# Kernel optimization log

Measured on AMD Instinct MI355X. Metric: run time of the kernel, lower is better.

Reference implementation:

```python
import jax, jax.numpy as jnp
import numpy as np

Nknn = 10
Np = 20
N = 524288
DOWN, LEFT, RIGHT, UP, WIDTH = -5.0, -5.0, 5.0, 5.0, 1.0


def setup_inputs() -> dict:
    key = jax.random.key(0)
    ks = jax.random.split(key, 20)
    def p(k, shape, fan_in):
        return jax.random.normal(k, shape, jnp.float32) / jnp.sqrt(jnp.float32(fan_in))
    inp = {
        "t": jax.random.uniform(ks[0], (1,), jnp.float32),
        "y": jax.random.normal(ks[1], (N, 4 + 2 * Np), jnp.float32),
        # net1: Linear(4,8) -> ReLU -> Linear(8,2)
        "w1a": p(ks[2], (4, 8), 4),   "b1a": p(ks[3], (8,), 4),
        "w1b": p(ks[4], (8, 2), 8),   "b1b": p(ks[5], (2,), 8),
        # net2: Linear(1,16) -> ReLU -> Linear(16,8) -> ReLU -> Linear(8,1)
        "w2a": p(ks[6], (1, 16), 1),  "b2a": p(ks[7], (16,), 1),
        "w2b": p(ks[8], (16, 8), 16), "b2b": p(ks[9], (8,), 16),
        "w2c": p(ks[10], (8, 1), 8),  "b2c": p(ks[11], (1,), 8),
        # net3: same architecture as net2
        "w3a": p(ks[12], (1, 16), 1), "b3a": p(ks[13], (16,), 1),
        "w3b": p(ks[14], (16, 8), 16),"b3b": p(ks[15], (8,), 16),
        "w3c": p(ks[16], (8, 1), 8),  "b3c": p(ks[17], (1,), 8),
    }
    return inp


def _mlp3(x, wa, ba, wb, bb, wc, bc):
    # Linear -> ReLU -> Linear -> ReLU -> Linear, applied on last axis
    h = jax.nn.relu(x @ wa + ba)
    h = jax.nn.relu(h @ wb + bb)
    return h @ wc + bc


def reference(t, y, w1a, b1a, w1b, b1b, w2a, b2a, w2b, b2b, w2c, b2c,
              w3a, b3a, w3b, b3b, w3c, b3c):
    y = y.astype(jnp.float32)
    theX = y[:, 0:2]            # positions [N,2]
    theV = y[:, 2:4]            # velocities [N,2]
    ux = y[:, 4:4 + 2 * Nknn].reshape(-1, Nknn, 2)  # neighbor offsets [N,Nknn,2]

    dxdt = theV

    # goal-attraction term f1
    door = jnp.array([RIGHT + 0.6, 0.0], jnp.float32)
    diff = door - theX
    unit_e = diff / jnp.sqrt(jnp.sum(diff * diff, axis=1, keepdims=True))
    h = jax.nn.relu(jnp.concatenate([unit_e, theV], axis=1) @ w1a + b1a)
    f1 = h @ w1b + b1b          # [N,2]

    # wall-repulsion term f2; rows inside the door gap get rightdist=100
    x0 = theX[:, 0:1]
    x1 = theX[:, 1:2]
    rightdist = jnp.where((x1 < WIDTH) & (x1 > -WIDTH), 100.0, RIGHT - x0)
    wall_in = jnp.stack([x0 - LEFT, x1 - DOWN, UP - x1, rightdist], axis=1)  # [N,4,1]
    o = _mlp3(wall_in, w2a, b2a, w2b, bb=b2b, wc=w2c, bc=b2c) if False else _mlp3(wall_in, w2a, b2a, w2b, b2b, w2c, b2c)  # [N,4,1]
    # directions: [1,0], [0,1], [0,-1], [-1,0]
    f2 = jnp.concatenate([o[:, 0] - o[:, 3], o[:, 1] - o[:, 2]], axis=1)  # [N,2]

    # neighbor-repulsion term f3 (vectorized over Nknn)
    d = jnp.sqrt(jnp.sum(ux * ux, axis=2, keepdims=True))  # [N,Nknn,1]
    f3 = -jnp.sum(_mlp3(d, w3a, b3a, w3b, b3b, w3c, b3c) * ux / d, axis=1)  # [N,2]

    dvdt = (f1 + f2 + f3) / 80.0
    dudt = jnp.zeros((y.shape[0], 2 * Nknn), y.dtype)
    result = jnp.concatenate([dxdt, dvdt, dudt], axis=1)  # [N, 4 + 2*Nknn]

    # zero out agents that have exited (x > RIGHT)
    result = jnp.where((theX[:, 0] > RIGHT)[:, None], 0.0, result)
    return result
```

## Files before the change

kernel.cpp:

```cpp
#include <hip/hip_runtime.h>

#define NROW  524288
#define BLK   256
#define TPB   2
#define NKNN  10
#define YCOLS 44
#define OCOLS 24

#define TBL    256
#define T2_LO  (-2.0f)
#define T3_LO  (0.0f)
#define T_H    (1.0f / 16.0f)
#define T_INVH 16.0f

typedef float f32x4 __attribute__((ext_vector_type(4)));

__device__ __forceinline__ float mlp_scalar_g(float s,
    const float* __restrict__ wa, const float* __restrict__ ba,
    const float* __restrict__ wb, const float* __restrict__ bb,
    const float* __restrict__ wc, const float* __restrict__ bc) {
    float h[16];
#pragma unroll
    for (int j = 0; j < 16; ++j)
        h[j] = fmaxf(fmaf(s, wa[j], ba[j]), 0.0f);
    float g[8];
#pragma unroll
    for (int k = 0; k < 8; ++k) g[k] = bb[k];
#pragma unroll
    for (int j = 0; j < 16; ++j) {
        float hj = h[j];
#pragma unroll
        for (int k = 0; k < 8; ++k)
            g[k] = fmaf(hj, wb[j * 8 + k], g[k]);
    }
    float o = bc[0];
#pragma unroll
    for (int k = 0; k < 8; ++k)
        o = fmaf(fmaxf(g[k], 0.0f), wc[k], o);
    return o;
}

__device__ __forceinline__ float tbl_eval(const float* __restrict__ T, float s, float lo) {
    float u = (s - lo) * T_INVH;
    u = fminf(fmaxf(u, 0.0f), (float)TBL - 1.001f);
    int i = (int)u;
    float f = u - (float)i;
    float va = T[i];
    float vb = T[i + 1];
    return fmaf(f, vb - va, va);
}

__device__ __forceinline__ void load_tile(const f32x4* __restrict__ yb,
                                          int w, int lane, f32x4 ld[6]) {
#pragma unroll
    for (int i = 0; i < 6; ++i) {
        int j  = lane + i * 64;
        int rr = j / 6;
        int cc = j - rr * 6;
        ld[i]  = yb[(64 * w + rr) * 11 + cc];
    }
}

__device__ __forceinline__ void stage_tile(f32x4* __restrict__ S,
                                           int w, int lane, const f32x4 ld[6]) {
#pragma unroll
    for (int i = 0; i < 6; ++i)
        S[384 * w + lane + i * 64] = ld[i];
}

__device__ __forceinline__ void compute_row(f32x4* __restrict__ S, int t,
    const float* __restrict__ T2v, const float* __restrict__ T3v, float o100,
    const float* __restrict__ w1a, const float* __restrict__ b1a,
    const float* __restrict__ w1b, const float* __restrict__ b1b)
{
    f32x4 a  = S[t * 6 + 0];
    f32x4 u0 = S[t * 6 + 1];
    f32x4 u1 = S[t * 6 + 2];
    f32x4 u2 = S[t * 6 + 3];
    f32x4 u3 = S[t * 6 + 4];
    f32x4 u4 = S[t * 6 + 5];

    float dx = 5.6f - a.x;
    float dy = 0.0f - a.y;
    float inv = rsqrtf(fmaf(dx, dx, dy * dy));
    float in1[4] = { dx * inv, dy * inv, a.z, a.w };
    float h1[8];
#pragma unroll
    for (int j = 0; j < 8; ++j) {
        float s = b1a[j];
#pragma unroll
        for (int k = 0; k < 4; ++k)
            s = fmaf(in1[k], w1a[k * 8 + j], s);
        h1[j] = fmaxf(s, 0.0f);
    }
    float f1x = b1b[0];
    float f1y = b1b[1];
#pragma unroll
    for (int j = 0; j < 8; ++j) {
        f1x = fmaf(h1[j], w1b[j * 2 + 0], f1x);
        f1y = fmaf(h1[j], w1b[j * 2 + 1], f1y);
    }

    bool corridor = (a.y < 1.0f) && (a.y > -1.0f);
    float o0 = tbl_eval(T2v, a.x + 5.0f, T2_LO);
    float o1 = tbl_eval(T2v, a.y + 5.0f, T2_LO);
    float o2 = tbl_eval(T2v, 5.0f - a.y, T2_LO);
    float o3 = corridor ? o100 : tbl_eval(T2v, 5.0f - a.x, T2_LO);
    float f2x = o0 - o3;
    float f2y = o1 - o2;

    float us[2 * NKNN] = { u0.x, u0.y, u0.z, u0.w,
                           u1.x, u1.y, u1.z, u1.w,
                           u2.x, u2.y, u2.z, u2.w,
                           u3.x, u3.y, u3.z, u3.w,
                           u4.x, u4.y, u4.z, u4.w };
    float f3x = 0.0f, f3y = 0.0f;
#pragma unroll
    for (int n = 0; n < NKNN; ++n) {
        float uxn = us[2 * n + 0];
        float uyn = us[2 * n + 1];
        float s2  = fmaf(uxn, uxn, uyn * uyn);
        float idn = rsqrtf(s2);
        float d   = s2 * idn;
        float m   = tbl_eval(T3v, d, T3_LO);
        float c   = m * idn;
        f3x = fmaf(-c, uxn, f3x);
        f3y = fmaf(-c, uyn, f3y);
    }

    bool dead = (a.x > 5.0f);
    const float k80 = 1.0f / 80.0f;
    f32x4 r;
    r.x = dead ? 0.0f : a.z;
    r.y = dead ? 0.0f : a.w;
    r.z = dead ? 0.0f : (f1x + f2x + f3x) * k80;
    r.w = dead ? 0.0f : (f1y + f2y + f3y) * k80;

    const f32x4 z = (f32x4)(0.0f);
    S[t * 6 + 0] = r;
    S[t * 6 + 1] = z;
    S[t * 6 + 2] = z;
    S[t * 6 + 3] = z;
    S[t * 6 + 4] = z;
    S[t * 6 + 5] = z;
}

__device__ __forceinline__ void store_tile(f32x4* __restrict__ ob,
                                           const f32x4* __restrict__ S,
                                           int w, int lane) {
#pragma unroll
    for (int i = 0; i < 6; ++i) {
        int j = 384 * w + lane + i * 64;
        f32x4 v = S[j];
        __builtin_nontemporal_store(v, &ob[j]);
    }
}

__global__ __launch_bounds__(BLK) void odefunc_kernel(
    const float* __restrict__ y,
    const float* __restrict__ w1a, const float* __restrict__ b1a,
    const float* __restrict__ w1b, const float* __restrict__ b1b,
    const float* __restrict__ w2a, const float* __restrict__ b2a,
    const float* __restrict__ w2b, const float* __restrict__ b2b,
    const float* __restrict__ w2c, const float* __restrict__ b2c,
    const float* __restrict__ w3a, const float* __restrict__ b3a,
    const float* __restrict__ w3b, const float* __restrict__ b3b,
    const float* __restrict__ w3c, const float* __restrict__ b3c,
    float* __restrict__ out)
{
    __shared__ f32x4 S[BLK * 6];
    __shared__ float T2v[TBL];
    __shared__ float T3v[TBL];
    __shared__ float o100s;

    const int t    = threadIdx.x;
    const int w    = t >> 6;
    const int lane = t & 63;

    const f32x4* yb0 = reinterpret_cast<const f32x4*>(y)
                     + (size_t)blockIdx.x * TPB * BLK * (YCOLS / 4);
    const f32x4* yb1 = yb0 + BLK * (YCOLS / 4);
    f32x4* ob0 = reinterpret_cast<f32x4*>(out)
               + (size_t)blockIdx.x * TPB * BLK * (OCOLS / 4);
    f32x4* ob1 = ob0 + BLK * (OCOLS / 4);

    f32x4 ld0[6];
    load_tile(yb0, w, lane, ld0);

    T2v[t] = mlp_scalar_g(T2_LO + (float)t * T_H, w2a, b2a, w2b, b2b, w2c, b2c);
    T3v[t] = mlp_scalar_g(T3_LO + (float)t * T_H, w3a, b3a, w3b, b3b, w3c, b3c);
    if (t == 0)
        o100s = mlp_scalar_g(100.0f, w2a, b2a, w2b, b2b, w2c, b2c);

    __syncthreads();
    const float o100 = o100s;

    stage_tile(S, w, lane, ld0);
    __builtin_amdgcn_wave_barrier();

    f32x4 ld1[6];
    load_tile(yb1, w, lane, ld1);

    compute_row(S, t, T2v, T3v, o100, w1a, b1a, w1b, b1b);
    __builtin_amdgcn_wave_barrier();
    store_tile(ob0, S, w, lane);
    __builtin_amdgcn_wave_barrier();

    stage_tile(S, w, lane, ld1);
    __builtin_amdgcn_wave_barrier();

    compute_row(S, t, T2v, T3v, o100, w1a, b1a, w1b, b1b);
    __builtin_amdgcn_wave_barrier();
    store_tile(ob1, S, w, lane);
}

extern "C" void kernel_launch(void* const* d_in, const int* in_sizes, int n_in,
                              void* d_out, int out_size, void* d_ws, size_t ws_size,
                              hipStream_t stream) {
    int iy = 1;
    for (int i = 0; i < n_in; ++i) {
        if (in_sizes[i] == NROW * YCOLS) { iy = i; break; }
    }
    const float* y   = (const float*)d_in[iy];
    const float* w1a = (const float*)d_in[iy + 1];
    const float* b1a = (const float*)d_in[iy + 2];
    const float* w1b = (const float*)d_in[iy + 3];
    const float* b1b = (const float*)d_in[iy + 4];
    const float* w2a = (const float*)d_in[iy + 5];
    const float* b2a = (const float*)d_in[iy + 6];
    const float* w2b = (const float*)d_in[iy + 7];
    const float* b2b = (const float*)d_in[iy + 8];
    const float* w2c = (const float*)d_in[iy + 9];
    const float* b2c = (const float*)d_in[iy + 10];
    const float* w3a = (const float*)d_in[iy + 11];
    const float* b3a = (const float*)d_in[iy + 12];
    const float* w3b = (const float*)d_in[iy + 13];
    const float* b3b = (const float*)d_in[iy + 14];
    const float* w3c = (const float*)d_in[iy + 15];
    const float* b3c = (const float*)d_in[iy + 16];
    float* out = (float*)d_out;

    hipLaunchKernelGGL(odefunc_kernel, dim3(NROW / (BLK * TPB)), dim3(BLK), 0, stream,
                       y, w1a, b1a, w1b, b1b,
                       w2a, b2a, w2b, b2b, w2c, b2c,
                       w3a, b3a, w3b, b3b, w3c, b3c, out);
}
```

Before: 28.57 us.

## Pad LDS rows to avoid bank conflicts and halve per-thread table build

Shared-memory staging now stores each row as scalar floats with a stride of 25, so each thread's row reads in compute_row avoid LDS bank conflicts. The zero output columns are produced in registers during the store rather than being written to and read back from LDS. The MLP lookup tables shrink to 128 entries with twice the grid step, so each thread evaluates one small MLP instead of two during setup. The coarser linear interpolation lowers accuracy and could approach the tolerance, and the scalar LDS stores add instructions.

Measured after the change: 25.90 us (median of 2 runs). -9.3%, faster.

```diff
diff --git a/kernel.cpp b/kernel.cpp
--- a/kernel.cpp
+++ b/kernel.cpp
@@ -7,11 +7,12 @@
 #define YCOLS 44
 #define OCOLS 24
 
-#define TBL    256
+#define TBL    128
 #define T2_LO  (-2.0f)
 #define T3_LO  (0.0f)
-#define T_H    (1.0f / 16.0f)
-#define T_INVH 16.0f
+#define T_H    (1.0f / 8.0f)
+#define T_INVH 8.0f
+#define SROW   25
 
 typedef float f32x4 __attribute__((ext_vector_type(4)));
 
@@ -61,29 +62,37 @@
     }
 }
 
-__device__ __forceinline__ void stage_tile(f32x4* __restrict__ S,
+__device__ __forceinline__ void stage_tile(float* __restrict__ Sf,
                                            int w, int lane, const f32x4 ld[6]) {
 #pragma unroll
-    for (int i = 0; i < 6; ++i)
-        S[384 * w + lane + i * 64] = ld[i];
-}
-
-__device__ __forceinline__ void compute_row(f32x4* __restrict__ S, int t,
+    for (int i = 0; i < 6; ++i) {
+        int j  = lane + i * 64;
+        int rr = j / 6;
+        int cc = j - rr * 6;
+        int base = (64 * w + rr) * SROW + 4 * cc;
+        Sf[base + 0] = ld[i].x;
+        Sf[base + 1] = ld[i].y;
+        Sf[base + 2] = ld[i].z;
+        Sf[base + 3] = ld[i].w;
+    }
+}
+
+__device__ __forceinline__ void compute_row(float* __restrict__ Sf, int t,
     const float* __restrict__ T2v, const float* __restrict__ T3v, float o100,
     const float* __restrict__ w1a, const float* __restrict__ b1a,
     const float* __restrict__ w1b, const float* __restrict__ b1b)
 {
-    f32x4 a  = S[t * 6 + 0];
-    f32x4 u0 = S[t * 6 + 1];
-    f32x4 u1 = S[t * 6 + 2];
-    f32x4 u2 = S[t * 6 + 3];
-    f32x4 u3 = S[t * 6 + 4];
-    f32x4 u4 = S[t * 6 + 5];
-
-    float dx = 5.6f - a.x;
-    float dy = 0.0f - a.y;
+    float* R = Sf + t * SROW;
+    float x0 = R[0], x1 = R[1], vx = R[2], vy = R[3];
+    float us[2 * NKNN];
+#pragma unroll
+    for (int m = 0; m < 2 * NKNN; ++m)
+        us[m] = R[4 + m];
+
+    float dx = 5.6f - x0;
+    float dy = 0.0f - x1;
     float inv = rsqrtf(fmaf(dx, dx, dy * dy));
-    float in1[4] = { dx * inv, dy * inv, a.z, a.w };
+    float in1[4] = { dx * inv, dy * inv, vx, vy };
     float h1[8];
 #pragma unroll
     for (int j = 0; j < 8; ++j) {
@@ -101,19 +110,14 @@
         f1y = fmaf(h1[j], w1b[j * 2 + 1], f1y);
     }
 
-    bool corridor = (a.y < 1.0f) && (a.y > -1.0f);
-    float o0 = tbl_eval(T2v, a.x + 5.0f, T2_LO);
-    float o1 = tbl_eval(T2v, a.y + 5.0f, T2_LO);
-    float o2 = tbl_eval(T2v, 5.0f - a.y, T2_LO);
-    float o3 = corridor ? o100 : tbl_eval(T2v, 5.0f - a.x, T2_LO);
+    bool corridor = (x1 < 1.0f) && (x1 > -1.0f);
+    float o0 = tbl_eval(T2v, x0 + 5.0f, T2_LO);
+    float o1 = tbl_eval(T2v, x1 + 5.0f, T2_LO);
+    float o2 = tbl_eval(T2v, 5.0f - x1, T2_LO);
+    float o3 = corridor ? o100 : tbl_eval(T2v, 5.0f - x0, T2_LO);
     float f2x = o0 - o3;
     float f2y = o1 - o2;
 
-    float us[2 * NKNN] = { u0.x, u0.y, u0.z, u0.w,
-                           u1.x, u1.y, u1.z, u1.w,
-                           u2.x, u2.y, u2.z, u2.w,
-                           u3.x, u3.y, u3.z, u3.w,
-                           u4.x, u4.y, u4.z, u4.w };
     float f3x = 0.0f, f3y = 0.0f;
 #pragma unroll
     for (int n = 0; n < NKNN; ++n) {
@@ -128,31 +132,28 @@
         f3y = fmaf(-c, uyn, f3y);
     }
 
-    bool dead = (a.x > 5.0f);
+    bool dead = (x0 > 5.0f);
     const float k80 = 1.0f / 80.0f;
-    f32x4 r;
-    r.x = dead ? 0.0f : a.z;
-    r.y = dead ? 0.0f : a.w;
-    r.z = dead ? 0.0f : (f1x + f2x + f3x) * k80;
-    r.w = dead ? 0.0f : (f1y + f2y + f3y) * k80;
-
-    const f32x4 z = (f32x4)(0.0f);
-    S[t * 6 + 0] = r;
-    S[t * 6 + 1] = z;
-    S[t * 6 + 2] = z;
-    S[t * 6 + 3] = z;
-    S[t * 6 + 4] = z;
-    S[t * 6 + 5] = z;
+    R[0] = dead ? 0.0f : vx;
+    R[1] = dead ? 0.0f : vy;
+    R[2] = dead ? 0.0f : (f1x + f2x + f3x) * k80;
+    R[3] = dead ? 0.0f : (f1y + f2y + f3y) * k80;
 }
 
 __device__ __forceinline__ void store_tile(f32x4* __restrict__ ob,
-                                           const f32x4* __restrict__ S,
+                                           const float* __restrict__ Sf,
                                            int w, int lane) {
 #pragma unroll
     for (int i = 0; i < 6; ++i) {
-        int j = 384 * w + lane + i * 64;
-        f32x4 v = S[j];
-        __builtin_nontemporal_store(v, &ob[j]);
+        int j  = lane + i * 64;
+        int rr = j / 6;
+        int cc = j - rr * 6;
+        f32x4 v = (f32x4)(0.0f);
+        if (cc == 0) {
+            const float* R = Sf + (64 * w + rr) * SROW;
+            v.x = R[0]; v.y = R[1]; v.z = R[2]; v.w = R[3];
+        }
+        __builtin_nontemporal_store(v, &ob[384 * w + j]);
     }
 }
 
@@ -168,7 +169,7 @@
     const float* __restrict__ w3c, const float* __restrict__ b3c,
     float* __restrict__ out)
 {
-    __shared__ f32x4 S[BLK * 6];
+    __shared__ float Sf[BLK * SROW];
     __shared__ float T2v[TBL];
     __shared__ float T3v[TBL];
     __shared__ float o100s;
@@ -187,31 +188,35 @@
     f32x4 ld0[6];
     load_tile(yb0, w, lane, ld0);
 
-    T2v[t] = mlp_scalar_g(T2_LO + (float)t * T_H, w2a, b2a, w2b, b2b, w2c, b2c);
-    T3v[t] = mlp_scalar_g(T3_LO + (float)t * T_H, w3a, b3a, w3b, b3b, w3c, b3c);
-    if (t == 0)
-        o100s = mlp_scalar_g(100.0f, w2a, b2a, w2b, b2b, w2c, b2c);
+    if (t < TBL) {
+        T2v[t] = mlp_scalar_g(T2_LO + (float)t * T_H, w2a, b2a, w2b, b2b, w2c, b2c);
+        if (t == 0)
+            o100s = mlp_scalar_g(100.0f, w2a, b2a, w2b, b2b, w2c, b2c);
+    } else {
+        int i3 = t - TBL;
+        T3v[i3] = mlp_scalar_g(T3_LO + (float)i3 * T_H, w3a, b3a, w3b, b3b, w3c, b3c);
+    }
 
     __syncthreads();
     const float o100 = o100s;
 
-    stage_tile(S, w, lane, ld0);
+    stage_tile(Sf, w, lane, ld0);
     __builtin_amdgcn_wave_barrier();
 
     f32x4 ld1[6];
     load_tile(yb1, w, lane, ld1);
 
-    compute_row(S, t, T2v, T3v, o100, w1a, b1a, w1b, b1b);
-    __builtin_amdgcn_wave_barrier();
-    store_tile(ob0, S, w, lane);
-    __builtin_amdgcn_wave_barrier();
-
-    stage_tile(S, w, lane, ld1);
-    __builtin_amdgcn_wave_barrier();
-
-    compute_row(S, t, T2v, T3v, o100, w1a, b1a, w1b, b1b);
-    __builtin_amdgcn_wave_barrier();
-    store_tile(ob1, S, w, lane);
+    compute_row(Sf, t, T2v, T3v, o100, w1a, b1a, w1b, b1b);
+    __builtin_amdgcn_wave_barrier();
+    store_tile(ob0, Sf, w, lane);
+    __builtin_amdgcn_wave_barrier();
+
+    stage_tile(Sf, w, lane, ld1);
+    __builtin_amdgcn_wave_barrier();
+
+    compute_row(Sf, t, T2v, T3v, o100, w1a, b1a, w1b, b1b);
+    __builtin_amdgcn_wave_barrier();
+    store_tile(ob1, Sf, w, lane);
 }
 
 extern "C" void kernel_launch(void* const* d_in, const int* in_sizes, int n_in,
```
